# Kernel optimization log

Measured on AMD Instinct MI355X. Metric: run time of the kernel, lower is better.

Reference implementation:

```python
import jax, jax.numpy as jnp
import numpy as np

LAMBDA_DEPTHG = 0.3
STEGO_TEMPERATURE = 0.1
KNN_K = 7
DEPTH_SIGMA = 0.5
EPS = 1e-8


def _l2norm(x):
    return x / jnp.sqrt(jnp.sum(x * x, axis=-1, keepdims=True) + EPS)


def _stego_loss(codes, feats, temperature, knn_k):
    # Pairwise cosine similarity of DINO features -> KNN graph (includes self).
    f = _l2norm(feats)                                  # (B,N,Df)
    sim_f = jnp.einsum('bnd,bmd->bnm', f, f)            # (B,N,N)
    _, knn_idx = jax.lax.top_k(sim_f, knn_k)            # (B,N,k) int32
    # Temperature-scaled InfoNCE over code similarities; KNN entries are positives.
    c = _l2norm(codes)                                  # (B,N,Dc)
    logits = jnp.einsum('bnd,bmd->bnm', c, c) / temperature  # (B,N,N)
    logp = jax.nn.log_softmax(logits, axis=-1)          # (B,N,N)
    pos_logp = jnp.take_along_axis(logp, knn_idx, axis=-1)   # (B,N,k)
    return -jnp.mean(pos_logp)


def _depth_guided_correlation_loss(codes, depth, sigma_d):
    # Gaussian depth affinity: pixels at similar depth should have similar codes.
    dd = depth[:, :, None] - depth[:, None, :]          # (B,N,N)
    w = jnp.exp(-(dd * dd) / (2.0 * sigma_d * sigma_d)) # (B,N,N)
    c = _l2norm(codes)
    s = jnp.einsum('bnd,bmd->bnm', c, c)                # (B,N,N) cosine corr
    return jnp.mean(w * (1.0 - s))


def setup_inputs() -> dict:
    key = jax.random.key(0)
    k1, k2, k3 = jax.random.split(key, 3)
    B, N = 2, 4096
    semantic_codes = jax.random.normal(k1, (B, N, 90), dtype=jnp.float32)
    dino_features = jax.random.normal(k2, (B, N, 384), dtype=jnp.float32)
    depth = jax.random.uniform(k3, (B, N), dtype=jnp.float32)
    return {"semantic_codes": semantic_codes, "dino_features": dino_features, "depth": depth}


def reference(semantic_codes, dino_features, depth):
    l_stego = _stego_loss(semantic_codes, dino_features, STEGO_TEMPERATURE, KNN_K)
    l_depthg = _depth_guided_correlation_loss(semantic_codes, depth, DEPTH_SIGMA)
    total = l_stego + LAMBDA_DEPTHG * l_depthg
    return (l_stego, l_depthg, total)
```

## Files before the change

kernel.cpp:

```cpp
#include <hip/hip_runtime.h>
#include <math.h>

#define NPTS 4096

typedef __attribute__((ext_vector_type(8))) short bf16x8;
typedef __attribute__((ext_vector_type(16))) float f32x16;
typedef long fp8x8;

#define KEEP(x) asm volatile("" : "+v"(x))

__device__ __forceinline__ f32x16 zero16() {
  f32x16 z;
#pragma unroll
  for (int i = 0; i < 16; ++i) z[i] = 0.f;
  return z;
}

__device__ __forceinline__ unsigned packkey(float x, int m) {
  unsigned u = __float_as_uint(x);
  unsigned key = u ^ ((unsigned)((int)u >> 31) | 0x80000000u);
  return (key & 0xFFFFF000u) | (unsigned)m;
}

__device__ __forceinline__ void cas7(unsigned v, unsigned* s) {
#pragma unroll
  for (int t = 0; t < 7; ++t) {
    const unsigned hi = s[t] >= v ? s[t] : v;
    const unsigned lo = s[t] >= v ? v : s[t];
    s[t] = hi;
    v = lo;
  }
}

#define KSENT 0u

__device__ __forceinline__ unsigned bf16pack(float a, float b) {
  unsigned ua = __float_as_uint(a); ua = (ua + 0x7FFFu + ((ua >> 16) & 1u)) >> 16;
  unsigned ub = __float_as_uint(b); ub = (ub + 0x7FFFu + ((ub >> 16) & 1u)) >> 16;
  return ua | (ub << 16);
}

__global__ __launch_bounds__(64) void norm_all(const float* __restrict__ feats,
                                               const float* __restrict__ codes,
                                               unsigned char* __restrict__ Fsw8,
                                               unsigned short* __restrict__ Csw,
                                               float* __restrict__ invc) {
  const int row = blockIdx.x;
  const int lane = threadIdx.x;
  const int b = row >> 12, mt = (row >> 5) & 127, rl = row & 31;

  const float* f = feats + (size_t)row * 384;
  float v[8];
  float ss = 0.f;
  if (lane < 48) {
    float4 p0 = *(const float4*)(f + lane * 8);
    float4 p1 = *(const float4*)(f + lane * 8 + 4);
    v[0] = p0.x; v[1] = p0.y; v[2] = p0.z; v[3] = p0.w;
    v[4] = p1.x; v[5] = p1.y; v[6] = p1.z; v[7] = p1.w;
#pragma unroll
    for (int e = 0; e < 8; ++e) ss = fmaf(v[e], v[e], ss);
  }
#pragma unroll
  for (int m = 1; m <= 32; m <<= 1) ss += __shfl_xor(ss, m, 64);
  const float s8 = rsqrtf(ss + 1e-8f) * 8.0f;
  if (lane < 48) {
    int w0 = __builtin_amdgcn_cvt_pk_fp8_f32(v[0] * s8, v[1] * s8, 0, 0);
    w0 = __builtin_amdgcn_cvt_pk_fp8_f32(v[2] * s8, v[3] * s8, w0, 1);
    int w1 = __builtin_amdgcn_cvt_pk_fp8_f32(v[4] * s8, v[5] * s8, 0, 0);
    w1 = __builtin_amdgcn_cvt_pk_fp8_f32(v[6] * s8, v[7] * s8, w1, 1);
    const int kc = lane >> 1, hs = lane & 1;
    uint2 o = make_uint2((unsigned)w0, (unsigned)w1);
    *(uint2*)(Fsw8 + (((size_t)(b * 128 + mt) * 24 + kc) << 9) + (hs * 32 + rl) * 8) = o;
  }

  const float* c = codes + (size_t)row * 90;
  float cv[8];
#pragma unroll
  for (int e = 0; e < 8; ++e) cv[e] = 0.f;
  if (lane < 11) {
    float4 p0 = *(const float4*)(c + lane * 8);
    float4 p1 = *(const float4*)(c + lane * 8 + 4);
    cv[0] = p0.x; cv[1] = p0.y; cv[2] = p0.z; cv[3] = p0.w;
    cv[4] = p1.x; cv[5] = p1.y; cv[6] = p1.z; cv[7] = p1.w;
  } else if (lane == 11) {
    cv[0] = c[88]; cv[1] = c[89];
  }
  float cs = 0.f;
#pragma unroll
  for (int e = 0; e < 8; ++e) cs = fmaf(cv[e], cv[e], cs);
#pragma unroll
  for (int m = 1; m <= 32; m <<= 1) cs += __shfl_xor(cs, m, 64);
  const float cinv = rsqrtf(cs + 1e-8f);
  if (lane < 12) {
    uint4 o;
    o.x = bf16pack(cv[0] * cinv, cv[1] * cinv);
    o.y = bf16pack(cv[2] * cinv, cv[3] * cinv);
    o.z = bf16pack(cv[4] * cinv, cv[5] * cinv);
    o.w = bf16pack(cv[6] * cinv, cv[7] * cinv);
    const int kc = lane >> 1, hs = lane & 1;
    *(uint4*)(Csw + (((size_t)(b * 128 + mt) * 6 + kc) << 9) + (hs * 32 + rl) * 8) = o;
  }
  if (lane == 0) invc[row] = cinv;
}

__global__ __launch_bounds__(1024, 4) void knn_mfma(const unsigned char* __restrict__ Fsw8,
                                                    unsigned* __restrict__ cand) {
  __shared__ unsigned long long qfrag[24 * 64];
  __shared__ unsigned ckey[16][32][7];
  const int g = blockIdx.x;
  const int b = g & 1;
  const int qt = g >> 1;
  const int q0 = qt * 32;
  const int tid = threadIdx.x;
  const int w = tid >> 6;
  const int lane = tid & 63;
  const int lo = lane & 31, hi4 = (lane >> 5) * 4;
  const unsigned char* Fb = Fsw8 + (size_t)b * 128 * 24 * 512;

  {
    const unsigned long long* src =
        (const unsigned long long*)(Fb + ((size_t)qt * 24) * 512);
#pragma unroll
    for (int k = 0; k < 2; ++k) {
      const int i = tid + k * 1024;
      if (i < 24 * 64) qfrag[i] = src[i];
    }
  }
  __syncthreads();

  unsigned s7[7];
#pragma unroll
  for (int t = 0; t < 7; ++t) s7[t] = KSENT;

  const int t0 = w * 8;
  const unsigned char* ab = Fb + ((size_t)t0 * 24) * 512 + lane * 8;

  fp8x8 a0[12], a1[12], bq[12];
#pragma unroll
  for (int t = 0; t < 12; ++t) a0[t] = *(const fp8x8*)(ab + t * 512);
#pragma unroll
  for (int t = 0; t < 12; ++t) KEEP(a0[t]);

  for (int mt = 0; mt < 8; ++mt) {
    const unsigned char* art = ab + (size_t)mt * 24 * 512;
#pragma unroll
    for (int t = 0; t < 12; ++t) a1[t] = *(const fp8x8*)(art + (12 + t) * 512);
#pragma unroll
    for (int t = 0; t < 12; ++t) KEEP(a1[t]);
#pragma unroll
    for (int t = 0; t < 12; ++t) bq[t] = (fp8x8)qfrag[t * 64 + lane];
#pragma unroll
    for (int t = 0; t < 12; ++t) KEEP(bq[t]);
    f32x16 acc = zero16();
#pragma unroll
    for (int t = 0; t < 12; ++t)
      acc = __builtin_amdgcn_mfma_f32_32x32x16_fp8_fp8(a0[t], bq[t], acc, 0, 0, 0);
    if (mt + 1 < 8) {
      const unsigned char* arn = ab + (size_t)(mt + 1) * 24 * 512;
#pragma unroll
      for (int t = 0; t < 12; ++t) a0[t] = *(const fp8x8*)(arn + t * 512);
#pragma unroll
      for (int t = 0; t < 12; ++t) KEEP(a0[t]);
    }
#pragma unroll
    for (int t = 0; t < 12; ++t) bq[t] = (fp8x8)qfrag[(12 + t) * 64 + lane];
#pragma unroll
    for (int t = 0; t < 12; ++t) KEEP(bq[t]);
#pragma unroll
    for (int t = 0; t < 12; ++t)
      acc = __builtin_amdgcn_mfma_f32_32x32x16_fp8_fp8(a1[t], bq[t], acc, 0, 0, 0);
    const int mb = (t0 + mt) * 32 + hi4;
#pragma unroll
    for (int r = 0; r < 16; ++r) {
      const int m = mb + (r & 3) + 8 * (r >> 2);
      cas7(packkey(acc[r], m), s7);
    }
  }

#pragma unroll
  for (int t = 0; t < 7; ++t) {
    const unsigned ov = (unsigned)__shfl_xor((int)s7[t], 32, 64);
    cas7(ov, s7);
  }
  if (lane < 32) {
#pragma unroll
    for (int t = 0; t < 7; ++t) ckey[w][lo][t] = s7[t];
  }
  __syncthreads();

  if (tid < 32) {
    unsigned fs[7];
#pragma unroll
    for (int t = 0; t < 7; ++t) fs[t] = KSENT;
    for (int w2 = 0; w2 < 16; ++w2)
#pragma unroll
      for (int t = 0; t < 7; ++t) cas7(ckey[w2][tid][t], fs);
    unsigned* o = cand + ((size_t)(b * NPTS) + q0 + tid) * 7;
#pragma unroll
    for (int t = 0; t < 7; ++t) o[t] = fs[t];
  }
}

__global__ __launch_bounds__(1024, 4) void lse_depth(const unsigned short* __restrict__ Csw,
                                                     const float* __restrict__ depth,
                                                     float* __restrict__ lse_out,
                                                     float* __restrict__ dpart) {
  __shared__ float lsep[16][32];
  __shared__ float depp[16];
  const int g = blockIdx.x;
  const int b = g & 1;
  const int qt = g >> 1;
  const int q0 = qt * 32;
  const int tid = threadIdx.x;
  const int w = tid >> 6;
  const int lane = tid & 63;
  const int lo = lane & 31, hi4 = (lane >> 5) * 4;
  const unsigned short* Cb = Csw + (size_t)b * 128 * 6 * 512;
  const float* db = depth + b * NPTS;

  bf16x8 bfr[6];
  {
    const unsigned short* qb = Cb + ((size_t)qt * 6) * 512 + lane * 8;
#pragma unroll
    for (int t = 0; t < 6; ++t) bfr[t] = *(const bf16x8*)(qb + t * 512);
#pragma unroll
    for (int t = 0; t < 6; ++t) KEEP(bfr[t]);
  }
  const float dq = db[q0 + lo];
  float slse = 0.f, sdep = 0.f;

  const int t0 = w * 8;
  const unsigned short* ab = Cb + ((size_t)t0 * 6) * 512 + lane * 8;

  bf16x8 a0[6], a1[6];
#pragma unroll
  for (int t = 0; t < 6; ++t) a0[t] = *(const bf16x8*)(ab + t * 512);
#pragma unroll
  for (int t = 0; t < 6; ++t) KEEP(a0[t]);

#define PROC3(A, GT)                                                           \
  {                                                                            \
    f32x16 acc = zero16();                                                     \
    _Pragma("unroll")                                                          \
    for (int t = 0; t < 6; ++t)                                                \
      acc = __builtin_amdgcn_mfma_f32_32x32x16_bf16(A[t], bfr[t], acc, 0, 0, 0); \
    float dvv[16];                                                             \
    _Pragma("unroll")                                                          \
    for (int k = 0; k < 4; ++k) {                                              \
      float4 dv = *(const float4*)(db + (GT) * 32 + hi4 + 8 * k);              \
      dvv[k * 4 + 0] = dv.x; dvv[k * 4 + 1] = dv.y;                            \
      dvv[k * 4 + 2] = dv.z; dvv[k * 4 + 3] = dv.w;                            \
    }                                                                          \
    _Pragma("unroll")                                                          \
    for (int r = 0; r < 16; ++r) {                                             \
      const float s = acc[r];                                                  \
      const float dd = dq - dvv[r];                                            \
      sdep += __expf(-2.f * dd * dd) * (1.f - s);                              \
      slse += __expf(fmaf(s, 10.f, -10.f));                                    \
    }                                                                          \
  }

  for (int mt = 0; mt < 8; mt += 2) {
    {
      const unsigned short* ar = ab + (size_t)(mt + 1) * 6 * 512;
#pragma unroll
      for (int t = 0; t < 6; ++t) a1[t] = *(const bf16x8*)(ar + t * 512);
#pragma unroll
      for (int t = 0; t < 6; ++t) KEEP(a1[t]);
    }
    PROC3(a0, t0 + mt)
    if (mt + 2 < 8) {
      const unsigned short* ar = ab + (size_t)(mt + 2) * 6 * 512;
#pragma unroll
      for (int t = 0; t < 6; ++t) a0[t] = *(const bf16x8*)(ar + t * 512);
#pragma unroll
      for (int t = 0; t < 6; ++t) KEEP(a0[t]);
    }
    PROC3(a1, t0 + mt + 1)
  }
#undef PROC3

  slse += __shfl_xor(slse, 32, 64);
  if (lane < 32) lsep[w][lo] = slse;
#pragma unroll
  for (int m = 1; m <= 32; m <<= 1) sdep += __shfl_xor(sdep, m, 64);
  if (lane == 0) depp[w] = sdep;
  __syncthreads();
  if (tid < 32) {
    float tot = 0.f;
#pragma unroll
    for (int w2 = 0; w2 < 16; ++w2) tot += lsep[w2][tid];
    lse_out[(size_t)(b * NPTS) + q0 + tid] = 10.f + __logf(tot);
  }
  if (tid == 32) {
    float d = 0.f;
#pragma unroll
    for (int w2 = 0; w2 < 16; ++w2) d += depp[w2];
    dpart[g] = d;
  }
}

__global__ __launch_bounds__(64) void gather_pos(const float* __restrict__ codes,
                                                 const float* __restrict__ invc,
                                                 const unsigned* __restrict__ cand,
                                                 float* __restrict__ gpart) {
  const int n = blockIdx.x;
  const int b = n >> 12, q = n & 4095;
  const int lane = threadIdx.x;

  unsigned s[7];
  const unsigned* cp = cand + (size_t)n * 7;
#pragma unroll
  for (int t = 0; t < 7; ++t) s[t] = cp[t];
  bool has = false;
#pragma unroll
  for (int t = 0; t < 7; ++t) has = has || ((s[t] & 4095u) == (unsigned)q);
  if (!has) s[6] = (unsigned)q;

  const float* cn = codes + (size_t)n * 90;
  float2 a = make_float2(0.f, 0.f);
  if (lane < 45) a = *(const float2*)(cn + lane * 2);
  const float inva = invc[n];
  float ssum = 0.f;
#pragma unroll
  for (int k = 0; k < 7; ++k) {
    const int m = (int)(s[k] & 4095u);
    const float* cm = codes + ((size_t)(b << 12) + m) * 90;
    float2 bb = make_float2(0.f, 0.f);
    if (lane < 45) bb = *(const float2*)(cm + lane * 2);
    float p = fmaf(a.x, bb.x, a.y * bb.y);
#pragma unroll
    for (int w = 1; w <= 32; w <<= 1) p += __shfl_xor(p, w, 64);
    ssum += p * inva * invc[(b << 12) + m];
  }
  if (lane == 0) gpart[n] = ssum;
}

__global__ __launch_bounds__(256) void finalize(const float* __restrict__ lse_out,
                                                const float* __restrict__ gpart,
                                                const float* __restrict__ dpart,
                                                float* __restrict__ out) {
  const int tid = threadIdx.x;
  float s1 = 0.f, s2 = 0.f;
  for (int n = tid; n < 2 * NPTS; n += 256) {
    s1 += lse_out[n];
    s2 += gpart[n];
  }
  float s3 = dpart[tid];
  __shared__ float r1[256], r2[256], r3[256];
  r1[tid] = s1; r2[tid] = s2; r3[tid] = s3;
  __syncthreads();
  for (int s = 128; s > 0; s >>= 1) {
    if (tid < s) { r1[tid] += r1[tid + s]; r2[tid] += r2[tid + s]; r3[tid] += r3[tid + s]; }
    __syncthreads();
  }
  if (tid == 0) {
    const float l_st = (7.f * r1[0] - 10.f * r2[0]) / 57344.f;
    const float l_dp = r3[0] / 33554432.f;
    out[0] = l_st;
    out[1] = l_dp;
    out[2] = l_st + 0.3f * l_dp;
  }
}

extern "C" void kernel_launch(void* const* d_in, const int* in_sizes, int n_in,
                              void* d_out, int out_size, void* d_ws, size_t ws_size,
                              hipStream_t stream) {
  (void)in_sizes; (void)n_in; (void)out_size; (void)ws_size;
  const float* codes = (const float*)d_in[0];
  const float* feats = (const float*)d_in[1];
  const float* depth = (const float*)d_in[2];
  float* out = (float*)d_out;

  char* ws = (char*)d_ws;
  float*    invc      = (float*)ws;
  unsigned* cand      = (unsigned*)(ws + 32768);
  unsigned char*  Fsw8 = (unsigned char*)(ws + 262144);
  unsigned short* Csw  = (unsigned short*)(ws + 3407872);
  float*    lse_out   = (float*)(ws + 4980736);
  float*    dpart     = (float*)(ws + 5013504);
  float*    gpart     = (float*)(ws + 5014528);

  norm_all<<<2 * NPTS, 64, 0, stream>>>(feats, codes, Fsw8, Csw, invc);
  knn_mfma<<<256, 1024, 0, stream>>>(Fsw8, cand);
  lse_depth<<<256, 1024, 0, stream>>>(Csw, depth, lse_out, dpart);
  gather_pos<<<2 * NPTS, 64, 0, stream>>>(codes, invc, cand, gpart);
  finalize<<<1, 256, 0, stream>>>(lse_out, gpart, dpart, out);
}
```

Measured before the change: 88.80 us.

## Process two query tiles per KNN block and split keys across block halves

Each knn_mfma block now handles 64 queries (two 32-query fragments in LDS) against half of the key range, reusing each loaded A fragment for two MFMA accumulators. Partial top-7 candidate lists for the two key halves are written separately, and gather_pos merges them. This halves the global key-fragment traffic per query and gives more MFMA work per load, at the cost of more registers (two accumulators and two sorted lists) and dropping the occupancy hint. The KEEP barriers in lse_depth are also moved to allow loads to overlap compute, and the workspace layout grows to hold the doubled candidate buffer.

New measurement: 84.78 us, median of 3. 4.5% less time.

```diff
diff --git a/kernel.cpp b/kernel.cpp
--- a/kernel.cpp
+++ b/kernel.cpp
@@ -103,14 +103,15 @@
   if (lane == 0) invc[row] = cinv;
 }
 
-__global__ __launch_bounds__(1024, 4) void knn_mfma(const unsigned char* __restrict__ Fsw8,
-                                                    unsigned* __restrict__ cand) {
-  __shared__ unsigned long long qfrag[24 * 64];
-  __shared__ unsigned ckey[16][32][7];
+__global__ __launch_bounds__(1024) void knn_mfma(const unsigned char* __restrict__ Fsw8,
+                                                 unsigned* __restrict__ cand) {
+  __shared__ unsigned long long qfrag[2 * 24 * 64];
+  __shared__ unsigned ckey[16][64][7];
   const int g = blockIdx.x;
   const int b = g & 1;
-  const int qt = g >> 1;
-  const int q0 = qt * 32;
+  const int h = (g >> 1) & 1;
+  const int qp = g >> 2;
+  const int q0 = qp * 64;
   const int tid = threadIdx.x;
   const int w = tid >> 6;
   const int lane = tid & 63;
@@ -119,92 +120,97 @@
 
   {
     const unsigned long long* src =
-        (const unsigned long long*)(Fb + ((size_t)qt * 24) * 512);
-#pragma unroll
-    for (int k = 0; k < 2; ++k) {
-      const int i = tid + k * 1024;
-      if (i < 24 * 64) qfrag[i] = src[i];
-    }
+        (const unsigned long long*)(Fb + ((size_t)(qp * 2) * 24) * 512);
+#pragma unroll
+    for (int k = 0; k < 3; ++k) qfrag[tid + k * 1024] = src[tid + k * 1024];
   }
   __syncthreads();
 
-  unsigned s7[7];
-#pragma unroll
-  for (int t = 0; t < 7; ++t) s7[t] = KSENT;
-
-  const int t0 = w * 8;
+  unsigned s7a[7], s7b[7];
+#pragma unroll
+  for (int t = 0; t < 7; ++t) { s7a[t] = KSENT; s7b[t] = KSENT; }
+
+  const int t0 = h * 64 + w * 4;
   const unsigned char* ab = Fb + ((size_t)t0 * 24) * 512 + lane * 8;
 
   fp8x8 a0[12], a1[12], bq[12];
 #pragma unroll
   for (int t = 0; t < 12; ++t) a0[t] = *(const fp8x8*)(ab + t * 512);
-#pragma unroll
-  for (int t = 0; t < 12; ++t) KEEP(a0[t]);
-
-  for (int mt = 0; mt < 8; ++mt) {
+
+  for (int mt = 0; mt < 4; ++mt) {
     const unsigned char* art = ab + (size_t)mt * 24 * 512;
 #pragma unroll
     for (int t = 0; t < 12; ++t) a1[t] = *(const fp8x8*)(art + (12 + t) * 512);
+    f32x16 acc0 = zero16(), acc1 = zero16();
+#pragma unroll
+    for (int t = 0; t < 12; ++t) bq[t] = (fp8x8)qfrag[t * 64 + lane];
+#pragma unroll
+    for (int t = 0; t < 12; ++t)
+      acc0 = __builtin_amdgcn_mfma_f32_32x32x16_fp8_fp8(a0[t], bq[t], acc0, 0, 0, 0);
+#pragma unroll
+    for (int t = 0; t < 12; ++t) bq[t] = (fp8x8)qfrag[1536 + t * 64 + lane];
+#pragma unroll
+    for (int t = 0; t < 12; ++t)
+      acc1 = __builtin_amdgcn_mfma_f32_32x32x16_fp8_fp8(a0[t], bq[t], acc1, 0, 0, 0);
 #pragma unroll
     for (int t = 0; t < 12; ++t) KEEP(a1[t]);
-#pragma unroll
-    for (int t = 0; t < 12; ++t) bq[t] = (fp8x8)qfrag[t * 64 + lane];
-#pragma unroll
-    for (int t = 0; t < 12; ++t) KEEP(bq[t]);
-    f32x16 acc = zero16();
+    if (mt + 1 < 4) {
+      const unsigned char* arn = ab + (size_t)(mt + 1) * 24 * 512;
+#pragma unroll
+      for (int t = 0; t < 12; ++t) a0[t] = *(const fp8x8*)(arn + t * 512);
+    }
+#pragma unroll
+    for (int t = 0; t < 12; ++t) bq[t] = (fp8x8)qfrag[(12 + t) * 64 + lane];
 #pragma unroll
     for (int t = 0; t < 12; ++t)
-      acc = __builtin_amdgcn_mfma_f32_32x32x16_fp8_fp8(a0[t], bq[t], acc, 0, 0, 0);
-    if (mt + 1 < 8) {
-      const unsigned char* arn = ab + (size_t)(mt + 1) * 24 * 512;
-#pragma unroll
-      for (int t = 0; t < 12; ++t) a0[t] = *(const fp8x8*)(arn + t * 512);
-#pragma unroll
-      for (int t = 0; t < 12; ++t) KEEP(a0[t]);
-    }
-#pragma unroll
-    for (int t = 0; t < 12; ++t) bq[t] = (fp8x8)qfrag[(12 + t) * 64 + lane];
-#pragma unroll
-    for (int t = 0; t < 12; ++t) KEEP(bq[t]);
+      acc0 = __builtin_amdgcn_mfma_f32_32x32x16_fp8_fp8(a1[t], bq[t], acc0, 0, 0, 0);
+#pragma unroll
+    for (int t = 0; t < 12; ++t) bq[t] = (fp8x8)qfrag[1536 + (12 + t) * 64 + lane];
 #pragma unroll
     for (int t = 0; t < 12; ++t)
-      acc = __builtin_amdgcn_mfma_f32_32x32x16_fp8_fp8(a1[t], bq[t], acc, 0, 0, 0);
+      acc1 = __builtin_amdgcn_mfma_f32_32x32x16_fp8_fp8(a1[t], bq[t], acc1, 0, 0, 0);
     const int mb = (t0 + mt) * 32 + hi4;
 #pragma unroll
     for (int r = 0; r < 16; ++r) {
       const int m = mb + (r & 3) + 8 * (r >> 2);
-      cas7(packkey(acc[r], m), s7);
+      cas7(packkey(acc0[r], m), s7a);
+      cas7(packkey(acc1[r], m), s7b);
     }
   }
 
 #pragma unroll
   for (int t = 0; t < 7; ++t) {
-    const unsigned ov = (unsigned)__shfl_xor((int)s7[t], 32, 64);
-    cas7(ov, s7);
+    const unsigned ova = (unsigned)__shfl_xor((int)s7a[t], 32, 64);
+    const unsigned ovb = (unsigned)__shfl_xor((int)s7b[t], 32, 64);
+    cas7(ova, s7a);
+    cas7(ovb, s7b);
   }
   if (lane < 32) {
 #pragma unroll
-    for (int t = 0; t < 7; ++t) ckey[w][lo][t] = s7[t];
+    for (int t = 0; t < 7; ++t) {
+      ckey[w][lo][t] = s7a[t];
+      ckey[w][32 + lo][t] = s7b[t];
+    }
   }
   __syncthreads();
 
-  if (tid < 32) {
+  if (tid < 64) {
     unsigned fs[7];
 #pragma unroll
     for (int t = 0; t < 7; ++t) fs[t] = KSENT;
     for (int w2 = 0; w2 < 16; ++w2)
 #pragma unroll
       for (int t = 0; t < 7; ++t) cas7(ckey[w2][tid][t], fs);
-    unsigned* o = cand + ((size_t)(b * NPTS) + q0 + tid) * 7;
+    unsigned* o = cand + ((size_t)((h * 2 + b) * NPTS) + q0 + tid) * 7;
 #pragma unroll
     for (int t = 0; t < 7; ++t) o[t] = fs[t];
   }
 }
 
-__global__ __launch_bounds__(1024, 4) void lse_depth(const unsigned short* __restrict__ Csw,
-                                                     const float* __restrict__ depth,
-                                                     float* __restrict__ lse_out,
-                                                     float* __restrict__ dpart) {
+__global__ __launch_bounds__(1024) void lse_depth(const unsigned short* __restrict__ Csw,
+                                                  const float* __restrict__ depth,
+                                                  float* __restrict__ lse_out,
+                                                  float* __restrict__ dpart) {
   __shared__ float lsep[16][32];
   __shared__ float depp[16];
   const int g = blockIdx.x;
@@ -265,18 +271,20 @@
       const unsigned short* ar = ab + (size_t)(mt + 1) * 6 * 512;
 #pragma unroll
       for (int t = 0; t < 6; ++t) a1[t] = *(const bf16x8*)(ar + t * 512);
-#pragma unroll
-      for (int t = 0; t < 6; ++t) KEEP(a1[t]);
     }
     PROC3(a0, t0 + mt)
+#pragma unroll
+    for (int t = 0; t < 6; ++t) KEEP(a1[t]);
     if (mt + 2 < 8) {
       const unsigned short* ar = ab + (size_t)(mt + 2) * 6 * 512;
 #pragma unroll
       for (int t = 0; t < 6; ++t) a0[t] = *(const bf16x8*)(ar + t * 512);
+    }
+    PROC3(a1, t0 + mt + 1)
+    if (mt + 2 < 8) {
 #pragma unroll
       for (int t = 0; t < 6; ++t) KEEP(a0[t]);
     }
-    PROC3(a1, t0 + mt + 1)
   }
 #undef PROC3
 
@@ -309,9 +317,14 @@
   const int lane = threadIdx.x;
 
   unsigned s[7];
-  const unsigned* cp = cand + (size_t)n * 7;
-#pragma unroll
-  for (int t = 0; t < 7; ++t) s[t] = cp[t];
+#pragma unroll
+  for (int t = 0; t < 7; ++t) s[t] = KSENT;
+  const unsigned* c0 = cand + ((size_t)(b * NPTS) + q) * 7;
+  const unsigned* c1 = cand + ((size_t)((2 + b) * NPTS) + q) * 7;
+#pragma unroll
+  for (int t = 0; t < 7; ++t) cas7(c0[t], s);
+#pragma unroll
+  for (int t = 0; t < 7; ++t) cas7(c1[t], s);
   bool has = false;
 #pragma unroll
   for (int t = 0; t < 7; ++t) has = has || ((s[t] & 4095u) == (unsigned)q);
@@ -375,11 +388,11 @@
   char* ws = (char*)d_ws;
   float*    invc      = (float*)ws;
   unsigned* cand      = (unsigned*)(ws + 32768);
-  unsigned char*  Fsw8 = (unsigned char*)(ws + 262144);
-  unsigned short* Csw  = (unsigned short*)(ws + 3407872);
-  float*    lse_out   = (float*)(ws + 4980736);
-  float*    dpart     = (float*)(ws + 5013504);
-  float*    gpart     = (float*)(ws + 5014528);
+  unsigned char*  Fsw8 = (unsigned char*)(ws + 491520);
+  unsigned short* Csw  = (unsigned short*)(ws + 3637248);
+  float*    lse_out   = (float*)(ws + 5210112);
+  float*    dpart     = (float*)(ws + 5242880);
+  float*    gpart     = (float*)(ws + 5243904);
 
   norm_all<<<2 * NPTS, 64, 0, stream>>>(feats, codes, Fsw8, Csw, invc);
   knn_mfma<<<256, 1024, 0, stream>>>(Fsw8, cand);
```
